# Performance work log

Hardware: AMD Instinct MI355X
Metric: run time of the kernel (lower is better)

The kernel has to match this reference:

```python
import jax, jax.numpy as jnp
import numpy as np

B, T, D = 8, 128, 256


def setup_inputs() -> dict:
    key = jax.random.key(0)
    k1, k2 = jax.random.split(key)
    dec_t = jax.random.normal(k1, (B, D), dtype=jnp.float32)
    enc_out = jax.random.normal(k2, (B, T, D), dtype=jnp.float32)
    return {"dec_t": dec_t, "enc_out": enc_out}


def reference(dec_t, enc_out):
    # Faithful vectorization of the original double Python loop.
    # Per timestep t: E[b,p,q] = exp(dec_t[b,p] * enc_out[b,t,q])  (outer product)
    # a_ts[b,p,q] = E[b,p,q] / rowsum[b,q]   (torch broadcast [D,D]/[D] divides
    #               each column q by the row-sum of row q: rowsum[q]=sum_r E[q,r])
    # contribution to c_t: a_ts[b,p,q] * enc_out[b,t,q], accumulated over t,
    # then summed over p.
    # => c_t[b,q] = sum_t enc_out[b,t,q] * colsum[b,t,q] / rowsum[b,t,q]
    E = jnp.exp(dec_t[:, None, :, None] * enc_out[:, :, None, :])  # [B,T,D,D]
    colsum = E.sum(axis=2)  # sum over p -> [B,T,D] indexed by q
    rowsum = E.sum(axis=3)  # sum over r -> [B,T,D] indexed by q (row q of outer)
    return jnp.sum(enc_out * colsum / rowsum, axis=1)  # [B,D]
```

## Files before the change

kernel.cpp:

```cpp
#include <hip/hip_runtime.h>

#define BB 8
#define TT 128
#define DD 256
#define LOG2E 1.44269504088896340736f

__global__ __launch_bounds__(256, 4) void attn_sym_kernel(
    const float* __restrict__ dec,
    const float* __restrict__ enc,
    float* __restrict__ ws) {
    const int blk = blockIdx.x;
    const int b = blk >> 7;
    const int tid = threadIdx.x;

    const float* __restrict__ drow = dec + b * DD;
    const float* __restrict__ erow = enc + blk * DD;

    const float dv = drow[tid];
    const float ev = erow[tid];
    const float dl2 = dv * LOG2E;
    const float el2 = ev * LOG2E;

    float cs0 = 0.f, cs1 = 0.f, cs2 = 0.f, cs3 = 0.f;
    float rs0 = 0.f, rs1 = 0.f, rs2 = 0.f, rs3 = 0.f;
    #pragma unroll 8
    for (int k = 0; k < DD; k += 4) {
        float4 d4 = *reinterpret_cast<const float4*>(drow + k);
        float4 e4 = *reinterpret_cast<const float4*>(erow + k);
        cs0 += __builtin_amdgcn_exp2f(d4.x * el2);
        cs1 += __builtin_amdgcn_exp2f(d4.y * el2);
        cs2 += __builtin_amdgcn_exp2f(d4.z * el2);
        cs3 += __builtin_amdgcn_exp2f(d4.w * el2);
        rs0 += __builtin_amdgcn_exp2f(dl2 * e4.x);
        rs1 += __builtin_amdgcn_exp2f(dl2 * e4.y);
        rs2 += __builtin_amdgcn_exp2f(dl2 * e4.z);
        rs3 += __builtin_amdgcn_exp2f(dl2 * e4.w);
    }
    const float cs = (cs0 + cs1) + (cs2 + cs3);
    const float rs = (rs0 + rs1) + (rs2 + rs3);

    ws[blk * DD + tid] = ev * cs / rs;
}

__global__ __launch_bounds__(256) void reduce_t_kernel(
    const float* __restrict__ ws, float* __restrict__ out) {
    __shared__ float red[4][64];
    const int b = blockIdx.x >> 2;
    const int qc = blockIdx.x & 3;
    const int qlane = threadIdx.x & 63;
    const int tc = threadIdx.x >> 6;
    const int q = qc * 64 + qlane;

    const float* p = ws + (b * TT + tc * 32) * DD + q;
    float a0 = 0.f, a1 = 0.f, a2 = 0.f, a3 = 0.f;
    #pragma unroll
    for (int t = 0; t < 32; t += 4) {
        a0 += p[(t + 0) * DD];
        a1 += p[(t + 1) * DD];
        a2 += p[(t + 2) * DD];
        a3 += p[(t + 3) * DD];
    }
    red[tc][qlane] = (a0 + a1) + (a2 + a3);
    __syncthreads();
    if (tc == 0)
        out[b * DD + q] = red[0][qlane] + red[1][qlane] +
                          red[2][qlane] + red[3][qlane];
}

extern "C" void kernel_launch(void* const* d_in, const int* in_sizes, int n_in,
                              void* d_out, int out_size, void* d_ws, size_t ws_size,
                              hipStream_t stream) {
    const float* dec = (const float*)d_in[0];
    const float* enc = (const float*)d_in[1];
    float* out = (float*)d_out;
    float* ws = (float*)d_ws;

    attn_sym_kernel<<<BB * TT, 256, 0, stream>>>(dec, enc, ws);
    reduce_t_kernel<<<BB * 4, 256, 0, stream>>>(ws, out);
}
```

Before: 70.36 us.

## Split exp-sum over two half-blocks and broadcast operands via ds_bpermute

The main kernel now launches twice as many blocks, and each block sums the exponentials over only half of the k dimension. The row operands are broadcast across lanes with ds_bpermute instead of float4 global/L1 loads. The partial column and row sums go to a workspace four times larger, and the reduce kernel combines them with enc, divides, and sums over t. The goal is more parallelism and lower load pressure, at the cost of extra workspace traffic and a reduce kernel that does more serial work. Because each wave of 64 lanes only broadcasts values from its own lanes, the loop over i<64 reads only the same 64-lane slice of indices. That slice is hb+l for lane l, so it does appear to cover the half correctly.

```diff
diff --git a/kernel.cpp b/kernel.cpp
--- a/kernel.cpp
+++ b/kernel.cpp
@@ -3,47 +3,54 @@
 #define BB 8
 #define TT 128
 #define DD 256
+#define BT (BB * TT)
+#define SZ (BT * DD)
 #define LOG2E 1.44269504088896340736f
 
-__global__ __launch_bounds__(256, 4) void attn_sym_kernel(
+__global__ __launch_bounds__(256, 8) void attn_part_kernel(
     const float* __restrict__ dec,
     const float* __restrict__ enc,
     float* __restrict__ ws) {
-    const int blk = blockIdx.x;
-    const int b = blk >> 7;
+    const int blk = blockIdx.x >> 1;
+    const int h   = blockIdx.x & 1;
+    const int b   = blk >> 7;
     const int tid = threadIdx.x;
+    const int l   = tid & 63;
 
     const float* __restrict__ drow = dec + b * DD;
     const float* __restrict__ erow = enc + blk * DD;
 
-    const float dv = drow[tid];
-    const float ev = erow[tid];
-    const float dl2 = dv * LOG2E;
-    const float el2 = ev * LOG2E;
+    const float el2 = erow[tid] * LOG2E;
+    const float dl2 = drow[tid] * LOG2E;
 
-    float cs0 = 0.f, cs1 = 0.f, cs2 = 0.f, cs3 = 0.f;
-    float rs0 = 0.f, rs1 = 0.f, rs2 = 0.f, rs3 = 0.f;
-    #pragma unroll 8
-    for (int k = 0; k < DD; k += 4) {
-        float4 d4 = *reinterpret_cast<const float4*>(drow + k);
-        float4 e4 = *reinterpret_cast<const float4*>(erow + k);
-        cs0 += __builtin_amdgcn_exp2f(d4.x * el2);
-        cs1 += __builtin_amdgcn_exp2f(d4.y * el2);
-        cs2 += __builtin_amdgcn_exp2f(d4.z * el2);
-        cs3 += __builtin_amdgcn_exp2f(d4.w * el2);
-        rs0 += __builtin_amdgcn_exp2f(dl2 * e4.x);
-        rs1 += __builtin_amdgcn_exp2f(dl2 * e4.y);
-        rs2 += __builtin_amdgcn_exp2f(dl2 * e4.z);
-        rs3 += __builtin_amdgcn_exp2f(dl2 * e4.w);
+    const int hb = h * 128;
+    const int dv0 = __float_as_int(drow[hb + l]);
+    const int dv1 = __float_as_int(drow[hb + 64 + l]);
+    const int ev0 = __float_as_int(erow[hb + l]);
+    const int ev1 = __float_as_int(erow[hb + 64 + l]);
+
+    float cs0 = 0.f, cs1 = 0.f, rs0 = 0.f, rs1 = 0.f;
+    #pragma unroll 4
+    for (int i = 0; i < 64; ++i) {
+        const int a = i << 2;
+        const float d0 = __int_as_float(__builtin_amdgcn_ds_bpermute(a, dv0));
+        const float d1 = __int_as_float(__builtin_amdgcn_ds_bpermute(a, dv1));
+        const float e0 = __int_as_float(__builtin_amdgcn_ds_bpermute(a, ev0));
+        const float e1 = __int_as_float(__builtin_amdgcn_ds_bpermute(a, ev1));
+        cs0 += __builtin_amdgcn_exp2f(d0 * el2);
+        cs1 += __builtin_amdgcn_exp2f(d1 * el2);
+        rs0 += __builtin_amdgcn_exp2f(dl2 * e0);
+        rs1 += __builtin_amdgcn_exp2f(dl2 * e1);
     }
-    const float cs = (cs0 + cs1) + (cs2 + cs3);
-    const float rs = (rs0 + rs1) + (rs2 + rs3);
 
-    ws[blk * DD + tid] = ev * cs / rs;
+    const int o = blk * DD + tid;
+    ws[h * SZ + o]       = cs0 + cs1;
+    ws[(2 + h) * SZ + o] = rs0 + rs1;
 }
 
 __global__ __launch_bounds__(256) void reduce_t_kernel(
-    const float* __restrict__ ws, float* __restrict__ out) {
+    const float* __restrict__ ws, const float* __restrict__ enc,
+    float* __restrict__ out) {
     __shared__ float red[4][64];
     const int b = blockIdx.x >> 2;
     const int qc = blockIdx.x & 3;
@@ -51,14 +58,18 @@
     const int tc = threadIdx.x >> 6;
     const int q = qc * 64 + qlane;
 
-    const float* p = ws + (b * TT + tc * 32) * DD + q;
+    const int base = (b * TT + tc * 32) * DD + q;
     float a0 = 0.f, a1 = 0.f, a2 = 0.f, a3 = 0.f;
-    #pragma unroll
+    #pragma unroll 4
     for (int t = 0; t < 32; t += 4) {
-        a0 += p[(t + 0) * DD];
-        a1 += p[(t + 1) * DD];
-        a2 += p[(t + 2) * DD];
-        a3 += p[(t + 3) * DD];
+        const int i0 = base + (t + 0) * DD;
+        const int i1 = base + (t + 1) * DD;
+        const int i2 = base + (t + 2) * DD;
+        const int i3 = base + (t + 3) * DD;
+        a0 += enc[i0] * (ws[i0] + ws[SZ + i0]) / (ws[2 * SZ + i0] + ws[3 * SZ + i0]);
+        a1 += enc[i1] * (ws[i1] + ws[SZ + i1]) / (ws[2 * SZ + i1] + ws[3 * SZ + i1]);
+        a2 += enc[i2] * (ws[i2] + ws[SZ + i2]) / (ws[2 * SZ + i2] + ws[3 * SZ + i2]);
+        a3 += enc[i3] * (ws[i3] + ws[SZ + i3]) / (ws[2 * SZ + i3] + ws[3 * SZ + i3]);
     }
     red[tc][qlane] = (a0 + a1) + (a2 + a3);
     __syncthreads();
@@ -75,6 +86,6 @@
     float* out = (float*)d_out;
     float* ws = (float*)d_ws;
 
-    attn_sym_kernel<<<BB * TT, 256, 0, stream>>>(dec, enc, ws);
-    reduce_t_kernel<<<BB * 4, 256, 0, stream>>>(ws, out);
+    attn_part_kernel<<<BT * 2, 256, 0, stream>>>(dec, enc, ws);
+    reduce_t_kernel<<<BB * 4, 256, 0, stream>>>(ws, enc, out);
 }
```

New measurement: 82.19 us. 1.17x slower.

## Compute each exp once per tile and reduce row and column sums via LDS

Applied to the files above, without the earlier changes.

Previously each thread recomputed exp for its column sum and, separately, for its row sum, so every element of the D×D outer-product exponential was evaluated twice. Now each thread owns a 16×16 tile and evaluates every exp exactly once, accumulating both partial column sums and partial row sums in registers. The partials are then combined through two LDS transpose-style reduction passes, which halves the exp work at the cost of extra shared memory, barriers and register pressure. The follow-up reduction over t is also retuned to launch more blocks with a finer split over t.

```diff
diff --git a/kernel.cpp b/kernel.cpp
--- a/kernel.cpp
+++ b/kernel.cpp
@@ -3,58 +3,96 @@
 #define BB 8
 #define TT 128
 #define DD 256
+#define BT (BB * TT)
 #define LOG2E 1.44269504088896340736f
 
-__global__ __launch_bounds__(256, 4) void attn_sym_kernel(
+__global__ __launch_bounds__(256, 4) void attn_tile_kernel(
     const float* __restrict__ dec,
     const float* __restrict__ enc,
     float* __restrict__ ws) {
     const int blk = blockIdx.x;
     const int b = blk >> 7;
     const int tid = threadIdx.x;
+    const int ti = tid >> 4;
+    const int tj = tid & 15;
 
     const float* __restrict__ drow = dec + b * DD;
     const float* __restrict__ erow = enc + blk * DD;
 
-    const float dv = drow[tid];
-    const float ev = erow[tid];
-    const float dl2 = dv * LOG2E;
-    const float el2 = ev * LOG2E;
+    float d[16], el2[16];
+    {
+        float4 v;
+        v = *reinterpret_cast<const float4*>(drow + ti * 16 + 0);
+        d[0] = v.x; d[1] = v.y; d[2] = v.z; d[3] = v.w;
+        v = *reinterpret_cast<const float4*>(drow + ti * 16 + 4);
+        d[4] = v.x; d[5] = v.y; d[6] = v.z; d[7] = v.w;
+        v = *reinterpret_cast<const float4*>(drow + ti * 16 + 8);
+        d[8] = v.x; d[9] = v.y; d[10] = v.z; d[11] = v.w;
+        v = *reinterpret_cast<const float4*>(drow + ti * 16 + 12);
+        d[12] = v.x; d[13] = v.y; d[14] = v.z; d[15] = v.w;
+        v = *reinterpret_cast<const float4*>(erow + tj * 16 + 0);
+        el2[0] = v.x * LOG2E; el2[1] = v.y * LOG2E; el2[2] = v.z * LOG2E; el2[3] = v.w * LOG2E;
+        v = *reinterpret_cast<const float4*>(erow + tj * 16 + 4);
+        el2[4] = v.x * LOG2E; el2[5] = v.y * LOG2E; el2[6] = v.z * LOG2E; el2[7] = v.w * LOG2E;
+        v = *reinterpret_cast<const float4*>(erow + tj * 16 + 8);
+        el2[8] = v.x * LOG2E; el2[9] = v.y * LOG2E; el2[10] = v.z * LOG2E; el2[11] = v.w * LOG2E;
+        v = *reinterpret_cast<const float4*>(erow + tj * 16 + 12);
+        el2[12] = v.x * LOG2E; el2[13] = v.y * LOG2E; el2[14] = v.z * LOG2E; el2[15] = v.w * LOG2E;
+    }
 
-    float cs0 = 0.f, cs1 = 0.f, cs2 = 0.f, cs3 = 0.f;
-    float rs0 = 0.f, rs1 = 0.f, rs2 = 0.f, rs3 = 0.f;
-    #pragma unroll 8
-    for (int k = 0; k < DD; k += 4) {
-        float4 d4 = *reinterpret_cast<const float4*>(drow + k);
-        float4 e4 = *reinterpret_cast<const float4*>(erow + k);
-        cs0 += __builtin_amdgcn_exp2f(d4.x * el2);
-        cs1 += __builtin_amdgcn_exp2f(d4.y * el2);
-        cs2 += __builtin_amdgcn_exp2f(d4.z * el2);
-        cs3 += __builtin_amdgcn_exp2f(d4.w * el2);
-        rs0 += __builtin_amdgcn_exp2f(dl2 * e4.x);
-        rs1 += __builtin_amdgcn_exp2f(dl2 * e4.y);
-        rs2 += __builtin_amdgcn_exp2f(dl2 * e4.z);
-        rs3 += __builtin_amdgcn_exp2f(dl2 * e4.w);
+    float cs[16], rs[16];
+    #pragma unroll
+    for (int q = 0; q < 16; ++q) { cs[q] = 0.f; rs[q] = 0.f; }
+    #pragma unroll
+    for (int p = 0; p < 16; ++p) {
+        const float dp = d[p];
+        #pragma unroll
+        for (int q = 0; q < 16; ++q) {
+            const float v = __builtin_amdgcn_exp2f(dp * el2[q]);
+            cs[q] += v;
+            rs[p] += v;
+        }
     }
-    const float cs = (cs0 + cs1) + (cs2 + cs3);
-    const float rs = (rs0 + rs1) + (rs2 + rs3);
 
-    ws[blk * DD + tid] = ev * cs / rs;
+    __shared__ float lds[256 * 16];
+    const int wbase = tid * 16;
+
+    *reinterpret_cast<float4*>(&lds[wbase + 0])  = make_float4(cs[0], cs[1], cs[2], cs[3]);
+    *reinterpret_cast<float4*>(&lds[wbase + 4])  = make_float4(cs[4], cs[5], cs[6], cs[7]);
+    *reinterpret_cast<float4*>(&lds[wbase + 8])  = make_float4(cs[8], cs[9], cs[10], cs[11]);
+    *reinterpret_cast<float4*>(&lds[wbase + 12]) = make_float4(cs[12], cs[13], cs[14], cs[15]);
+    __syncthreads();
+    float csum = 0.f;
+    #pragma unroll
+    for (int i2 = 0; i2 < 16; ++i2) csum += lds[i2 * 256 + tid];
+    __syncthreads();
+
+    *reinterpret_cast<float4*>(&lds[wbase + 0])  = make_float4(rs[0], rs[1], rs[2], rs[3]);
+    *reinterpret_cast<float4*>(&lds[wbase + 4])  = make_float4(rs[4], rs[5], rs[6], rs[7]);
+    *reinterpret_cast<float4*>(&lds[wbase + 8])  = make_float4(rs[8], rs[9], rs[10], rs[11]);
+    *reinterpret_cast<float4*>(&lds[wbase + 12]) = make_float4(rs[12], rs[13], rs[14], rs[15]);
+    __syncthreads();
+    float rsum = 0.f;
+    #pragma unroll
+    for (int j2 = 0; j2 < 16; ++j2)
+        rsum += lds[(tid >> 4) * 256 + j2 * 16 + (tid & 15)];
+
+    ws[blk * DD + tid] = erow[tid] * csum / rsum;
 }
 
 __global__ __launch_bounds__(256) void reduce_t_kernel(
     const float* __restrict__ ws, float* __restrict__ out) {
-    __shared__ float red[4][64];
-    const int b = blockIdx.x >> 2;
-    const int qc = blockIdx.x & 3;
-    const int qlane = threadIdx.x & 63;
-    const int tc = threadIdx.x >> 6;
-    const int q = qc * 64 + qlane;
+    __shared__ float red[8][32];
+    const int b = blockIdx.x >> 3;
+    const int qc = blockIdx.x & 7;
+    const int qlane = threadIdx.x & 31;
+    const int tc = threadIdx.x >> 5;
+    const int q = qc * 32 + qlane;
 
-    const float* p = ws + (b * TT + tc * 32) * DD + q;
+    const float* p = ws + (b * TT + tc * 16) * DD + q;
     float a0 = 0.f, a1 = 0.f, a2 = 0.f, a3 = 0.f;
     #pragma unroll
-    for (int t = 0; t < 32; t += 4) {
+    for (int t = 0; t < 16; t += 4) {
         a0 += p[(t + 0) * DD];
         a1 += p[(t + 1) * DD];
         a2 += p[(t + 2) * DD];
@@ -62,9 +100,12 @@
     }
     red[tc][qlane] = (a0 + a1) + (a2 + a3);
     __syncthreads();
-    if (tc == 0)
-        out[b * DD + q] = red[0][qlane] + red[1][qlane] +
-                          red[2][qlane] + red[3][qlane];
+    if (tc == 0) {
+        float s = 0.f;
+        #pragma unroll
+        for (int u = 0; u < 8; ++u) s += red[u][qlane];
+        out[b * DD + q] = s;
+    }
 }
 
 extern "C" void kernel_launch(void* const* d_in, const int* in_sizes, int n_in,
@@ -75,6 +116,6 @@
     float* out = (float*)d_out;
     float* ws = (float*)d_ws;
 
-    attn_sym_kernel<<<BB * TT, 256, 0, stream>>>(dec, enc, ws);
-    reduce_t_kernel<<<BB * 4, 256, 0, stream>>>(ws, out);
+    attn_tile_kernel<<<BT, 256, 0, stream>>>(dec, enc, ws);
+    reduce_t_kernel<<<BB * 8, 256, 0, stream>>>(ws, out);
 }
```

Measured after the change: 158.5 us. 2.25x slower.
